# Kernel optimization log

Hardware: AMD Instinct MI355X
Metric: run time of the kernel (lower is better)

## Reference

```python
import jax, jax.numpy as jnp
import numpy as np

D_MODEL = 512
NHEAD = 4
HEAD_DIM = D_MODEL // NHEAD


def setup_inputs() -> dict:
    key = jax.random.key(0)
    ks = jax.random.split(key, 12)
    B, S = 2, 4096
    s = 1.0 / np.sqrt(D_MODEL)
    inp = {
        "query": jax.random.normal(ks[0], (B, S, D_MODEL), jnp.float32),
        "key": jax.random.normal(ks[1], (B, S, D_MODEL), jnp.float32),
        "value": jax.random.normal(ks[2], (B, S, D_MODEL), jnp.float32),
        "Wq": jax.random.uniform(ks[3], (D_MODEL, D_MODEL), jnp.float32, -s, s),
        "bq": jax.random.uniform(ks[4], (D_MODEL,), jnp.float32, -s, s),
        "Wk": jax.random.uniform(ks[5], (D_MODEL, D_MODEL), jnp.float32, -s, s),
        "bk": jax.random.uniform(ks[6], (D_MODEL,), jnp.float32, -s, s),
        "Wv": jax.random.uniform(ks[7], (D_MODEL, D_MODEL), jnp.float32, -s, s),
        "bv": jax.random.uniform(ks[8], (D_MODEL,), jnp.float32, -s, s),
        "Wo": jax.random.uniform(ks[9], (D_MODEL, D_MODEL), jnp.float32, -s, s),
        "bo": jax.random.uniform(ks[10], (D_MODEL,), jnp.float32, -s, s),
    }
    return inp


def reference(query, key, value, Wq, bq, Wk, bk, Wv, bv, Wo, bo):
    B, Sq, _ = query.shape
    Sk = key.shape[1]
    # projections (torch Linear: x @ W.T + b); split heads -> [B, H, S, hd]
    def proj(x, W, b, S):
        return (x @ W.T + b).reshape(B, S, NHEAD, HEAD_DIM).transpose(0, 2, 1, 3)
    Q = proj(query, Wq, bq, Sq)
    K = proj(key, Wk, bk, Sk)
    V = proj(value, Wv, bv, Sk)
    scale = 1.0 / np.sqrt(HEAD_DIM).astype(np.float32)
    scores = jnp.einsum("bhqd,bhkd->bhqk", Q, K) * scale  # [B,H,Sq,Sk]
    weights = jax.nn.softmax(scores, axis=-1)
    out = jnp.einsum("bhqk,bhkd->bhqd", weights, V)  # [B,H,Sq,hd]
    out = out.transpose(0, 2, 1, 3).reshape(B, Sq, D_MODEL)
    return out @ Wo.T + bo
```

## Files before the change

kernel.cpp:

```cpp
#include <hip/hip_runtime.h>


#define D_MODEL 512
#define NHEAD 4
#define HD 128
#define S_ 4096

typedef __attribute__((ext_vector_type(8))) short bf16x8;
typedef __attribute__((ext_vector_type(4))) short bf16x4;
typedef __attribute__((ext_vector_type(4))) float f32x4;
typedef __attribute__((ext_vector_type(2))) unsigned uint2v;
typedef __attribute__((ext_vector_type(4))) unsigned uint4v;

#define SCQ (0.08838834764831845f * 1.4426950408889634f)

__device__ __forceinline__ short f2bf(float f) {
    unsigned u = __builtin_bit_cast(unsigned, f);
    u += 0x7fffu + ((u >> 16) & 1u);
    return (short)(u >> 16);
}
__device__ __forceinline__ unsigned pk2bf(float a, float b) {
    unsigned ua = __builtin_bit_cast(unsigned, a);
    ua += 0x7fffu + ((ua >> 16) & 1u);
    unsigned ub = __builtin_bit_cast(unsigned, b);
    ub += 0x7fffu + ((ub >> 16) & 1u);
    return (ua >> 16) | (ub & 0xffff0000u);
}
__device__ __forceinline__ void gl2lds16(const short* g, short* l) {
    __builtin_amdgcn_global_load_lds(
        (const __attribute__((address_space(1))) void*)g,
        (__attribute__((address_space(3))) void*)l, 16, 0, 0);
}

__global__ __launch_bounds__(256) void convert_kernel(
    const float* __restrict__ s0, const float* __restrict__ s1,
    const float* __restrict__ s2, const float* __restrict__ s3,
    const float* __restrict__ s4, const float* __restrict__ s5,
    const float* __restrict__ s6,
    short* __restrict__ d0, short* __restrict__ d1, short* __restrict__ d2,
    short* __restrict__ d3, short* __restrict__ d4, short* __restrict__ d5,
    short* __restrict__ d6)
{
    int seg = blockIdx.y;
    const float* src; short* dst; int n;
    const int NBIG = 2 * S_ * D_MODEL;
    const int NW = D_MODEL * D_MODEL;
    switch (seg) {
        case 0: src = s0; dst = d0; n = NBIG; break;
        case 1: src = s1; dst = d1; n = NBIG; break;
        case 2: src = s2; dst = d2; n = NBIG; break;
        case 3: src = s3; dst = d3; n = NW; break;
        case 4: src = s4; dst = d4; n = NW; break;
        case 5: src = s5; dst = d5; n = NW; break;
        default: src = s6; dst = d6; n = NW; break;
    }
    int idx = (blockIdx.x * 256 + threadIdx.x) * 8;
    if (idx >= n) return;
    float4 a = *(const float4*)(src + idx);
    float4 b = *(const float4*)(src + idx + 4);
    uint4v o;
    o[0] = pk2bf(a.x, a.y); o[1] = pk2bf(a.z, a.w);
    o[2] = pk2bf(b.x, b.y); o[3] = pk2bf(b.z, b.w);
    *(uint4v*)(dst + idx) = o;
}

__global__ __launch_bounds__(256) void qkv_kernel(
    const short* __restrict__ qb, const short* __restrict__ kb,
    const short* __restrict__ vb,
    const short* __restrict__ Wqb, const short* __restrict__ Wkb,
    const short* __restrict__ Wvb,
    const float* __restrict__ bq, const float* __restrict__ bk,
    const float* __restrict__ bv,
    short* __restrict__ Qh, short* __restrict__ Kh, short* __restrict__ VT)
{
    __shared__ short smem[12288];
    short* lA = smem;
    short* lB = smem + 4096;
    int z = blockIdx.z;
    const short* A    = (z == 0) ? qb  : (z == 1) ? kb  : vb;
    const short* W    = (z == 0) ? Wqb : (z == 1) ? Wkb : Wvb;
    const float* bias = (z == 0) ? bq  : (z == 1) ? bk  : bv;
    short* out        = (z == 0) ? Qh  : (z == 1) ? Kh  : VT;
    int vmode = (z == 2);
    float osc = (z == 0) ? SCQ : 1.0f;

    int t = threadIdx.x;
    int wv = t >> 6, ln = t & 63, q4 = ln >> 4, c = ln & 15;
    int m0 = blockIdx.x * 64, n0 = blockIdx.y * 128;
    f32x4 acc[8] = {};

    for (int k0 = 0; k0 < 512; k0 += 64) {
        for (int i = 0; i < 2; ++i) {
            int id = i * 256 + t;
            int m = id >> 3, kgp = id & 7;
            gl2lds16(A + (size_t)(m0 + m) * 512 + k0 + ((kgp ^ (m & 7)) << 3),
                     &lA[id * 8]);
        }
        for (int i = 0; i < 4; ++i) {
            int id = i * 256 + t;
            int n = id >> 3, kgp = id & 7;
            gl2lds16(W + (size_t)(n0 + n) * 512 + k0 + ((kgp ^ (n & 7)) << 3),
                     &lB[id * 8]);
        }
        __syncthreads();
        for (int ks = 0; ks < 2; ++ks) {
            int kg = ks * 4 + q4;
            int m = wv * 16 + c;
            bf16x8 af = *(bf16x8*)&lA[m * 64 + ((kg ^ (m & 7)) << 3)];
            bf16x8 bfr[8];
            for (int nt = 0; nt < 8; ++nt) {
                int n = nt * 16 + c;
                bfr[nt] = *(bf16x8*)&lB[n * 64 + ((kg ^ (n & 7)) << 3)];
            }
            for (int nt = 0; nt < 8; ++nt)
                acc[nt] = __builtin_amdgcn_mfma_f32_16x16x32_bf16(af, bfr[nt], acc[nt], 0, 0, 0);
        }
        __syncthreads();
    }

    if (vmode == 0) {
        const int TS = 136;
        short* lT = smem;
        for (int nt = 0; nt < 8; ++nt) {
            float bv_ = bias[n0 + nt * 16 + c];
            for (int r = 0; r < 4; ++r) {
                int srow = wv * 16 + q4 * 4 + r;
                lT[srow * TS + nt * 16 + c] = f2bf((acc[nt][r] + bv_) * osc);
            }
        }
        __syncthreads();
        int bb = m0 >> 12, sbase = m0 & 4095, h = blockIdx.y;
        for (int i = 0; i < 4; ++i) {
            int id = i * 256 + t;
            int row = id >> 4, g = id & 15;
            bf16x8 vv = *(bf16x8*)&lT[row * TS + g * 8];
            *(bf16x8*)&out[((size_t)((bb * NHEAD + h) * S_ + sbase + row)) * HD + g * 8] = vv;
        }
    } else {
        for (int nt = 0; nt < 8; ++nt) {
            int d = nt * 16 + c;
            float bv_ = bias[n0 + d];
            uint2v pv;
            pv[0] = pk2bf(acc[nt][0] + bv_, acc[nt][1] + bv_);
            pv[1] = pk2bf(acc[nt][2] + bv_, acc[nt][3] + bv_);
            int gr = wv * 4 + q4;
            *(uint2v*)&lB[d * 64 + ((gr ^ (d & 15)) << 2)] = pv;
        }
        __syncthreads();
        int bb = m0 >> 12, sbase = m0 & 4095, h = blockIdx.y;
        for (int i = 0; i < 8; ++i) {
            int id = i * 256 + t;
            int d = id >> 4, grl = id & 15;
            bf16x4 v = *(bf16x4*)&lB[d * 64 + ((grl ^ (d & 15)) << 2)];
            *(bf16x4*)&out[((size_t)((bb * NHEAD + h) * HD + d)) * S_ + sbase + grl * 4] = v;
        }
    }
}

__global__ __launch_bounds__(256) void outproj_kernel(
    const short* __restrict__ A, const short* __restrict__ W,
    const float* __restrict__ bias, float* __restrict__ out)
{
    __shared__ short lA[64 * 64];
    __shared__ short lB[128 * 64];
    int t = threadIdx.x;
    int wv = t >> 6, ln = t & 63, q4 = ln >> 4, c = ln & 15;
    int m0 = blockIdx.x * 64, n0 = blockIdx.y * 128;
    f32x4 acc[8] = {};

    for (int k0 = 0; k0 < 512; k0 += 64) {
        for (int i = 0; i < 2; ++i) {
            int id = i * 256 + t;
            int m = id >> 3, kgp = id & 7;
            gl2lds16(A + (size_t)(m0 + m) * 512 + k0 + ((kgp ^ (m & 7)) << 3),
                     &lA[id * 8]);
        }
        for (int i = 0; i < 4; ++i) {
            int id = i * 256 + t;
            int n = id >> 3, kgp = id & 7;
            gl2lds16(W + (size_t)(n0 + n) * 512 + k0 + ((kgp ^ (n & 7)) << 3),
                     &lB[id * 8]);
        }
        __syncthreads();
        for (int ks = 0; ks < 2; ++ks) {
            int kg = ks * 4 + q4;
            int m = wv * 16 + c;
            bf16x8 af = *(bf16x8*)&lA[m * 64 + ((kg ^ (m & 7)) << 3)];
            bf16x8 bfr[8];
            for (int nt = 0; nt < 8; ++nt) {
                int n = nt * 16 + c;
                bfr[nt] = *(bf16x8*)&lB[n * 64 + ((kg ^ (n & 7)) << 3)];
            }
            for (int nt = 0; nt < 8; ++nt)
                acc[nt] = __builtin_amdgcn_mfma_f32_16x16x32_bf16(af, bfr[nt], acc[nt], 0, 0, 0);
        }
        __syncthreads();
    }

    for (int nt = 0; nt < 8; ++nt) {
        int col = n0 + nt * 16 + c;
        float bv_ = bias[col];
        for (int r = 0; r < 4; ++r) {
            int mrow = m0 + wv * 16 + q4 * 4 + r;
            out[(size_t)mrow * 512 + col] = acc[nt][r] + bv_;
        }
    }
}

__global__ __launch_bounds__(256, 2) void flash_kernel(
    const short* __restrict__ Qh, const short* __restrict__ Kh,
    const short* __restrict__ VTg, short* __restrict__ AO,
    float* __restrict__ U, float* __restrict__ ML, int nsplit, int kkspan)
{
    __shared__ short lK[2][64 * 128];
    __shared__ short lVT[128 * 64];
    int t = threadIdx.x;
    int wv = t >> 6, ln = t & 63, q4 = ln >> 4, c = ln & 15;
    int bh = blockIdx.x;
    int s0 = blockIdx.y * 128;
    int z = blockIdx.z;
    const size_t base = (size_t)bh * S_ * HD;

    bf16x8 qf[2][4];
    #pragma unroll
    for (int qt = 0; qt < 2; ++qt) {
        int s = s0 + wv * 32 + qt * 16 + c;
        const short* qp = Qh + base + (size_t)s * HD + q4 * 8;
        #pragma unroll
        for (int ks = 0; ks < 4; ++ks)
            qf[qt][ks] = *(const bf16x8*)(qp + ks * 32);
    }

    f32x4 of[8][2] = {};
    float lrun[2] = {};

    int kkbeg = z * kkspan;
    int nt = kkspan >> 6;

    #pragma unroll
    for (int i = 0; i < 4; ++i) {
        int id = i * 256 + t;
        int m = id >> 4, kgp = id & 15;
        gl2lds16(Kh + base + (size_t)(kkbeg + m) * HD + ((kgp ^ (m & 7)) << 3),
                 &lK[0][id * 8]);
    }
    #pragma unroll
    for (int i = 0; i < 4; ++i) {
        int id = i * 256 + t;
        int mv = id >> 3, kgvp = id & 7;
        gl2lds16(VTg + base + (size_t)mv * S_ + kkbeg + ((kgvp ^ (mv & 7)) << 3),
                 &lVT[id * 8]);
    }
    asm volatile("s_waitcnt vmcnt(4)" ::: "memory");
    __builtin_amdgcn_s_barrier();
    __builtin_amdgcn_sched_barrier(0);

    int cur = 0;
    for (int it = 0; it < nt; ++it) {
        int kk0 = kkbeg + it * 64;
        int more = (it + 1 < nt);

        if (more) {
            #pragma unroll
            for (int i = 0; i < 4; ++i) {
                int id = i * 256 + t;
                int m = id >> 4, kgp = id & 15;
                gl2lds16(Kh + base + (size_t)(kk0 + 64 + m) * HD + ((kgp ^ (m & 7)) << 3),
                         &lK[cur ^ 1][id * 8]);
            }
        }

        f32x4 sf[2][4] = {};
        __builtin_amdgcn_s_setprio(1);
        #pragma unroll
        for (int ks = 0; ks < 4; ++ks) {
            int kg = ks * 4 + q4;
            bf16x8 af[4];
            #pragma unroll
            for (int kt = 0; kt < 4; ++kt) {
                int row = kt * 16 + c;
                af[kt] = *(bf16x8*)&lK[cur][row * 128 + ((kg ^ (row & 7)) << 3)];
            }
            #pragma unroll
            for (int qt = 0; qt < 2; ++qt)
                #pragma unroll
                for (int kt = 0; kt < 4; ++kt)
                    sf[qt][kt] = __builtin_amdgcn_mfma_f32_16x16x32_bf16(
                        af[kt], qf[qt][ks], sf[qt][kt], 0, 0, 0);
        }
        __builtin_amdgcn_s_setprio(0);

        bf16x8 bp[2][2];
        #pragma unroll
        for (int qt = 0; qt < 2; ++qt) {
            unsigned dlo[4], dhi[4];
            float lt = 0.f;
            #pragma unroll
            for (int kt = 0; kt < 4; ++kt) {
                float p0 = exp2f(sf[qt][kt][0]);
                float p1 = exp2f(sf[qt][kt][1]);
                float p2 = exp2f(sf[qt][kt][2]);
                float p3 = exp2f(sf[qt][kt][3]);
                lt += (p0 + p1) + (p2 + p3);
                asm("v_cvt_pk_bf16_f32 %0, %1, %2" : "=v"(dlo[kt]) : "v"(p0), "v"(p1));
                asm("v_cvt_pk_bf16_f32 %0, %1, %2" : "=v"(dhi[kt]) : "v"(p2), "v"(p3));
            }
            lrun[qt] += lt;
            #pragma unroll
            for (int ksv = 0; ksv < 2; ++ksv) {
                unsigned x0 = dlo[2 * ksv], y0 = dlo[2 * ksv + 1];
                unsigned x1 = dhi[2 * ksv], y1 = dhi[2 * ksv + 1];
                asm("v_permlane32_swap_b32 %0, %1" : "+v"(x0), "+v"(y0));
                asm("v_permlane16_swap_b32 %0, %1" : "+v"(x0), "+v"(y0));
                asm("v_permlane32_swap_b32 %0, %1" : "+v"(x1), "+v"(y1));
                asm("v_permlane16_swap_b32 %0, %1" : "+v"(x1), "+v"(y1));
                uint4v u; u[0] = x0; u[1] = x1; u[2] = y0; u[3] = y1;
                bp[qt][ksv] = __builtin_bit_cast(bf16x8, u);
            }
        }

        if (more) asm volatile("s_waitcnt vmcnt(4)" ::: "memory");
        else      asm volatile("s_waitcnt vmcnt(0)" ::: "memory");
        __builtin_amdgcn_s_barrier();
        __builtin_amdgcn_sched_barrier(0);

        __builtin_amdgcn_s_setprio(1);
        #pragma unroll
        for (int ksv = 0; ksv < 2; ++ksv) {
            int kg = ksv * 4 + q4;
            bf16x8 av[8];
            #pragma unroll
            for (int dt = 0; dt < 8; ++dt) {
                int row = dt * 16 + c;
                av[dt] = *(bf16x8*)&lVT[row * 64 + ((kg ^ (row & 7)) << 3)];
            }
            #pragma unroll
            for (int qt = 0; qt < 2; ++qt)
                #pragma unroll
                for (int dt = 0; dt < 8; ++dt)
                    of[dt][qt] = __builtin_amdgcn_mfma_f32_16x16x32_bf16(
                        av[dt], bp[qt][ksv], of[dt][qt], 0, 0, 0);
        }
        __builtin_amdgcn_s_setprio(0);

        asm volatile("s_waitcnt vmcnt(0)" ::: "memory");
        __builtin_amdgcn_s_barrier();
        __builtin_amdgcn_sched_barrier(0);

        if (more) {
            #pragma unroll
            for (int i = 0; i < 4; ++i) {
                int id = i * 256 + t;
                int mv = id >> 3, kgvp = id & 7;
                gl2lds16(VTg + base + (size_t)mv * S_ + kk0 + 64 + ((kgvp ^ (mv & 7)) << 3),
                         &lVT[id * 8]);
            }
        }
        cur ^= 1;
    }

    #pragma unroll
    for (int qt = 0; qt < 2; ++qt) {
        lrun[qt] += __shfl_xor(lrun[qt], 16);
        lrun[qt] += __shfl_xor(lrun[qt], 32);
    }

    if (nsplit > 1) {
        #pragma unroll
        for (int qt = 0; qt < 2; ++qt) {
            int s = s0 + wv * 32 + qt * 16 + c;
            size_t rowu = (size_t)(z * 8 + bh) * S_ + s;
            float* up = U + rowu * HD;
            #pragma unroll
            for (int dt = 0; dt < 8; ++dt)
                *(f32x4*)&up[dt * 16 + q4 * 4] = of[dt][qt];
            if (q4 == 0) ML[rowu] = lrun[qt];
        }
    } else {
        int b = bh >> 2, h = bh & 3;
        #pragma unroll
        for (int qt = 0; qt < 2; ++qt) {
            float inv = 1.0f / lrun[qt];
            int s = s0 + wv * 32 + qt * 16 + c;
            short* dst = AO + ((size_t)(b * S_ + s)) * D_MODEL + h * HD;
            #pragma unroll
            for (int dt = 0; dt < 8; ++dt) {
                uint2v ov;
                ov[0] = pk2bf(of[dt][qt][0] * inv, of[dt][qt][1] * inv);
                ov[1] = pk2bf(of[dt][qt][2] * inv, of[dt][qt][3] * inv);
                *(uint2v*)(dst + dt * 16 + q4 * 4) = ov;
            }
        }
    }
}

__global__ __launch_bounds__(256) void combine_kernel(
    const float* __restrict__ U, const float* __restrict__ ML,
    short* __restrict__ AO, int nsplit)
{
    int row = blockIdx.x * 8 + (threadIdx.x >> 5);
    int d4 = (threadIdx.x & 31) * 4;
    const int R = 8 * S_;
    float l = 0.f;
    f32x4 u = {0.f, 0.f, 0.f, 0.f};
    for (int zz = 0; zz < nsplit; ++zz) {
        l += ML[(size_t)zz * R + row];
        f32x4 uz = *(const f32x4*)&U[((size_t)zz * R + row) * HD + d4];
        u += uz;
    }
    float inv = 1.0f / l;
    uint2v o;
    o[0] = pk2bf(u[0] * inv, u[1] * inv);
    o[1] = pk2bf(u[2] * inv, u[3] * inv);
    int bh = row >> 12, s = row & 4095;
    int b = bh >> 2, h = bh & 3;
    *(uint2v*)&AO[((size_t)(b * S_ + s)) * D_MODEL + h * HD + d4] = o;
}

extern "C" void kernel_launch(void* const* d_in, const int* in_sizes, int n_in,
                              void* d_out, int out_size, void* d_ws, size_t ws_size,
                              hipStream_t stream) {
    const float* q  = (const float*)d_in[0];
    const float* k  = (const float*)d_in[1];
    const float* v  = (const float*)d_in[2];
    const float* Wq = (const float*)d_in[3];
    const float* bq = (const float*)d_in[4];
    const float* Wk = (const float*)d_in[5];
    const float* bk = (const float*)d_in[6];
    const float* Wv = (const float*)d_in[7];
    const float* bv = (const float*)d_in[8];
    const float* Wo = (const float*)d_in[9];
    const float* bo = (const float*)d_in[10];

    const size_t HS = (size_t)2 * NHEAD * S_ * HD;
    const size_t NBIG = HS;
    const size_t NW = (size_t)D_MODEL * D_MODEL;
    const size_t R = (size_t)8 * S_;

    char* wsb = (char*)d_ws;
    short* Qh = (short*)wsb;
    short* Kh = Qh + HS;
    short* VT = Kh + HS;
    short* AO = VT + HS;
    char* r2 = wsb + 4 * HS * 2;
    short* qb  = (short*)r2;
    short* kb  = qb + NBIG;
    short* vb  = kb + NBIG;
    short* Wqb = vb + NBIG;
    short* Wkb = Wqb + NW;
    short* Wvb = Wkb + NW;
    float* U   = (float*)r2;

    int nsplit = 1;
    size_t r2sz = 3 * NBIG * 2 + 3 * NW * 2;
    for (int cand = 4; cand >= 2; cand -= 2) {
        size_t r2c = (size_t)cand * R * HD * 4;
        if (r2c < 3 * NBIG * 2 + 3 * NW * 2) r2c = 3 * NBIG * 2 + 3 * NW * 2;
        size_t need = 4 * HS * 2 + r2c + (size_t)cand * R * 4 + NW * 2;
        if (ws_size >= need) { nsplit = cand; r2sz = r2c; break; }
    }
    float* ML  = (float*)(r2 + r2sz);
    short* Wob = (short*)((char*)ML + (size_t)nsplit * R * 4);
    int kkspan = S_ / nsplit;

    dim3 blk(256);
    convert_kernel<<<dim3(2048, 7), blk, 0, stream>>>(
        q, k, v, Wq, Wk, Wv, Wo, qb, kb, vb, Wqb, Wkb, Wvb, Wob);
    qkv_kernel<<<dim3(128, 4, 3), blk, 0, stream>>>(
        qb, kb, vb, Wqb, Wkb, Wvb, bq, bk, bv, Qh, Kh, VT);
    flash_kernel<<<dim3(8, 32, nsplit), blk, 0, stream>>>(
        Qh, Kh, VT, AO, U, ML, nsplit, kkspan);
    if (nsplit > 1)
        combine_kernel<<<dim3(S_), blk, 0, stream>>>(U, ML, AO, nsplit);
    outproj_kernel<<<dim3(128, 4), blk, 0, stream>>>(AO, Wob, bo, (float*)d_out);
}
```

Baseline: 244.6 us.

## Double-buffer LDS in projection GEMMs and cap flash split-K at two

Result: faster. 228.4 us (-6.6%).

```diff
diff --git a/kernel.cpp b/kernel.cpp
--- a/kernel.cpp
+++ b/kernel.cpp
@@ -73,9 +73,7 @@
     const float* __restrict__ bv,
     short* __restrict__ Qh, short* __restrict__ Kh, short* __restrict__ VT)
 {
-    __shared__ short smem[12288];
-    short* lA = smem;
-    short* lB = smem + 4096;
+    __shared__ short smem[24576];
     int z = blockIdx.z;
     const short* A    = (z == 0) ? qb  : (z == 1) ? kb  : vb;
     const short* W    = (z == 0) ? Wqb : (z == 1) ? Wkb : Wvb;
@@ -89,33 +87,69 @@
     int m0 = blockIdx.x * 64, n0 = blockIdx.y * 128;
     f32x4 acc[8] = {};
 
-    for (int k0 = 0; k0 < 512; k0 += 64) {
+    {
+        short* lAd = smem;
+        short* lBd = smem + 8192;
+        #pragma unroll
         for (int i = 0; i < 2; ++i) {
             int id = i * 256 + t;
             int m = id >> 3, kgp = id & 7;
-            gl2lds16(A + (size_t)(m0 + m) * 512 + k0 + ((kgp ^ (m & 7)) << 3),
-                     &lA[id * 8]);
-        }
+            gl2lds16(A + (size_t)(m0 + m) * 512 + ((kgp ^ (m & 7)) << 3), &lAd[id * 8]);
+        }
+        #pragma unroll
         for (int i = 0; i < 4; ++i) {
             int id = i * 256 + t;
             int n = id >> 3, kgp = id & 7;
-            gl2lds16(W + (size_t)(n0 + n) * 512 + k0 + ((kgp ^ (n & 7)) << 3),
-                     &lB[id * 8]);
-        }
-        __syncthreads();
+            gl2lds16(W + (size_t)(n0 + n) * 512 + ((kgp ^ (n & 7)) << 3), &lBd[id * 8]);
+        }
+    }
+    asm volatile("s_waitcnt vmcnt(0)" ::: "memory");
+    __builtin_amdgcn_s_barrier();
+    __builtin_amdgcn_sched_barrier(0);
+
+    int cur = 0;
+    for (int k0 = 0; k0 < 512; k0 += 64) {
+        int more = (k0 < 448);
+        if (more) {
+            short* lAd = smem + (cur ^ 1) * 4096;
+            short* lBd = smem + 8192 + (cur ^ 1) * 8192;
+            int kn = k0 + 64;
+            #pragma unroll
+            for (int i = 0; i < 2; ++i) {
+                int id = i * 256 + t;
+                int m = id >> 3, kgp = id & 7;
+                gl2lds16(A + (size_t)(m0 + m) * 512 + kn + ((kgp ^ (m & 7)) << 3), &lAd[id * 8]);
+            }
+            #pragma unroll
+            for (int i = 0; i < 4; ++i) {
+                int id = i * 256 + t;
+                int n = id >> 3, kgp = id & 7;
+                gl2lds16(W + (size_t)(n0 + n) * 512 + kn + ((kgp ^ (n & 7)) << 3), &lBd[id * 8]);
+            }
+        }
+        short* lAc = smem + cur * 4096;
+        short* lBc = smem + 8192 + cur * 8192;
+        __builtin_amdgcn_s_setprio(1);
+        #pragma unroll
         for (int ks = 0; ks < 2; ++ks) {
             int kg = ks * 4 + q4;
             int m = wv * 16 + c;
-            bf16x8 af = *(bf16x8*)&lA[m * 64 + ((kg ^ (m & 7)) << 3)];
+            bf16x8 af = *(bf16x8*)&lAc[m * 64 + ((kg ^ (m & 7)) << 3)];
             bf16x8 bfr[8];
+            #pragma unroll
             for (int nt = 0; nt < 8; ++nt) {
                 int n = nt * 16 + c;
-                bfr[nt] = *(bf16x8*)&lB[n * 64 + ((kg ^ (n & 7)) << 3)];
-            }
+                bfr[nt] = *(bf16x8*)&lBc[n * 64 + ((kg ^ (n & 7)) << 3)];
+            }
+            #pragma unroll
             for (int nt = 0; nt < 8; ++nt)
                 acc[nt] = __builtin_amdgcn_mfma_f32_16x16x32_bf16(af, bfr[nt], acc[nt], 0, 0, 0);
         }
-        __syncthreads();
+        __builtin_amdgcn_s_setprio(0);
+        if (more) asm volatile("s_waitcnt vmcnt(0)" ::: "memory");
+        __builtin_amdgcn_s_barrier();
+        __builtin_amdgcn_sched_barrier(0);
+        cur ^= 1;
     }
 
     if (vmode == 0) {
@@ -137,6 +171,7 @@
             *(bf16x8*)&out[((size_t)((bb * NHEAD + h) * S_ + sbase + row)) * HD + g * 8] = vv;
         }
     } else {
+        short* lB0 = smem + 8192;
         for (int nt = 0; nt < 8; ++nt) {
             int d = nt * 16 + c;
             float bv_ = bias[n0 + d];
@@ -144,14 +179,14 @@
             pv[0] = pk2bf(acc[nt][0] + bv_, acc[nt][1] + bv_);
             pv[1] = pk2bf(acc[nt][2] + bv_, acc[nt][3] + bv_);
             int gr = wv * 4 + q4;
-            *(uint2v*)&lB[d * 64 + ((gr ^ (d & 15)) << 2)] = pv;
+            *(uint2v*)&lB0[d * 64 + ((gr ^ (d & 15)) << 2)] = pv;
         }
         __syncthreads();
         int bb = m0 >> 12, sbase = m0 & 4095, h = blockIdx.y;
         for (int i = 0; i < 8; ++i) {
             int id = i * 256 + t;
             int d = id >> 4, grl = id & 15;
-            bf16x4 v = *(bf16x4*)&lB[d * 64 + ((grl ^ (d & 15)) << 2)];
+            bf16x4 v = *(bf16x4*)&lB0[d * 64 + ((grl ^ (d & 15)) << 2)];
             *(bf16x4*)&out[((size_t)((bb * NHEAD + h) * HD + d)) * S_ + sbase + grl * 4] = v;
         }
     }
@@ -161,40 +196,75 @@
     const short* __restrict__ A, const short* __restrict__ W,
     const float* __restrict__ bias, float* __restrict__ out)
 {
-    __shared__ short lA[64 * 64];
-    __shared__ short lB[128 * 64];
+    __shared__ short smem[24576];
     int t = threadIdx.x;
     int wv = t >> 6, ln = t & 63, q4 = ln >> 4, c = ln & 15;
     int m0 = blockIdx.x * 64, n0 = blockIdx.y * 128;
     f32x4 acc[8] = {};
 
-    for (int k0 = 0; k0 < 512; k0 += 64) {
+    {
+        short* lAd = smem;
+        short* lBd = smem + 8192;
+        #pragma unroll
         for (int i = 0; i < 2; ++i) {
             int id = i * 256 + t;
             int m = id >> 3, kgp = id & 7;
-            gl2lds16(A + (size_t)(m0 + m) * 512 + k0 + ((kgp ^ (m & 7)) << 3),
-                     &lA[id * 8]);
-        }
+            gl2lds16(A + (size_t)(m0 + m) * 512 + ((kgp ^ (m & 7)) << 3), &lAd[id * 8]);
+        }
+        #pragma unroll
         for (int i = 0; i < 4; ++i) {
             int id = i * 256 + t;
             int n = id >> 3, kgp = id & 7;
-            gl2lds16(W + (size_t)(n0 + n) * 512 + k0 + ((kgp ^ (n & 7)) << 3),
-                     &lB[id * 8]);
-        }
-        __syncthreads();
+            gl2lds16(W + (size_t)(n0 + n) * 512 + ((kgp ^ (n & 7)) << 3), &lBd[id * 8]);
+        }
+    }
+    asm volatile("s_waitcnt vmcnt(0)" ::: "memory");
+    __builtin_amdgcn_s_barrier();
+    __builtin_amdgcn_sched_barrier(0);
+
+    int cur = 0;
+    for (int k0 = 0; k0 < 512; k0 += 64) {
+        int more = (k0 < 448);
+        if (more) {
+            short* lAd = smem + (cur ^ 1) * 4096;
+            short* lBd = smem + 8192 + (cur ^ 1) * 8192;
+            int kn = k0 + 64;
+            #pragma unroll
+            for (int i = 0; i < 2; ++i) {
+                int id = i * 256 + t;
+                int m = id >> 3, kgp = id & 7;
+                gl2lds16(A + (size_t)(m0 + m) * 512 + kn + ((kgp ^ (m & 7)) << 3), &lAd[id * 8]);
+            }
+            #pragma unroll
+            for (int i = 0; i < 4; ++i) {
+                int id = i * 256 + t;
+                int n = id >> 3, kgp = id & 7;
+                gl2lds16(W + (size_t)(n0 + n) * 512 + kn + ((kgp ^ (n & 7)) << 3), &lBd[id * 8]);
+            }
+        }
+        short* lAc = smem + cur * 4096;
+        short* lBc = smem + 8192 + cur * 8192;
+        __builtin_amdgcn_s_setprio(1);
+        #pragma unroll
         for (int ks = 0; ks < 2; ++ks) {
             int kg = ks * 4 + q4;
             int m = wv * 16 + c;
-            bf16x8 af = *(bf16x8*)&lA[m * 64 + ((kg ^ (m & 7)) << 3)];
+            bf16x8 af = *(bf16x8*)&lAc[m * 64 + ((kg ^ (m & 7)) << 3)];
             bf16x8 bfr[8];
+            #pragma unroll
             for (int nt = 0; nt < 8; ++nt) {
                 int n = nt * 16 + c;
-                bfr[nt] = *(bf16x8*)&lB[n * 64 + ((kg ^ (n & 7)) << 3)];
-            }
+                bfr[nt] = *(bf16x8*)&lBc[n * 64 + ((kg ^ (n & 7)) << 3)];
+            }
+            #pragma unroll
             for (int nt = 0; nt < 8; ++nt)
                 acc[nt] = __builtin_amdgcn_mfma_f32_16x16x32_bf16(af, bfr[nt], acc[nt], 0, 0, 0);
         }
-        __syncthreads();
+        __builtin_amdgcn_s_setprio(0);
+        if (more) asm volatile("s_waitcnt vmcnt(0)" ::: "memory");
+        __builtin_amdgcn_s_barrier();
+        __builtin_amdgcn_sched_barrier(0);
+        cur ^= 1;
     }
 
     for (int nt = 0; nt < 8; ++nt) {
@@ -453,11 +523,12 @@
 
     int nsplit = 1;
     size_t r2sz = 3 * NBIG * 2 + 3 * NW * 2;
-    for (int cand = 4; cand >= 2; cand -= 2) {
+    {
+        int cand = 2;
         size_t r2c = (size_t)cand * R * HD * 4;
         if (r2c < 3 * NBIG * 2 + 3 * NW * 2) r2c = 3 * NBIG * 2 + 3 * NW * 2;
         size_t need = 4 * HS * 2 + r2c + (size_t)cand * R * 4 + NW * 2;
-        if (ws_size >= need) { nsplit = cand; r2sz = r2c; break; }
+        if (ws_size >= need) { nsplit = cand; r2sz = r2c; }
     }
     float* ML  = (float*)(r2 + r2sz);
     short* Wob = (short*)((char*)ML + (size_t)nsplit * R * 4);
```
